# Performance work log

Measured on AMD Instinct MI355X. Metric: run time of the kernel, lower is better.

Reference implementation:

```python
import jax, jax.numpy as jnp
import numpy as np

NEG_SLOPE = 0.2  # PyG GATv2Conv default negative_slope


def _gatv2_layer(x, src, dst, Wl, Wr, att, bias, heads, out_ch, concat, num_nodes):
    # x: [N, F_in]; src/dst: [E'] (self-loops already appended)
    N, H, C = num_nodes, heads, out_ch
    xl = (x @ Wl).reshape(N, H, C)  # source-side transform (lin_l)
    xr = (x @ Wr).reshape(N, H, C)  # target-side transform (lin_r)
    m = xl[src] + xr[dst]                       # [E', H, C]
    e = jax.nn.leaky_relu(m, NEG_SLOPE)
    logits = jnp.einsum('ehc,hc->eh', e, att)   # [E', H]
    # numerically stable segment softmax over incoming edges of each dst node
    mx = jax.ops.segment_max(logits, dst, num_segments=N)   # [N, H]
    ex = jnp.exp(logits - mx[dst])
    den = jax.ops.segment_sum(ex, dst, num_segments=N)      # [N, H]
    alpha = ex / den[dst]                                    # [E', H]
    out = jax.ops.segment_sum(alpha[:, :, None] * xl[src], dst, num_segments=N)  # [N, H, C]
    out = out.reshape(N, H * C) if concat else out.mean(axis=1)
    return out + bias


def setup_inputs() -> dict:
    key = jax.random.key(0)
    N, E = 50000, 800000
    IN, HID, OUT, HEADS = 128, 32, 64, 4
    ks = jax.random.split(key, 16)
    x = jax.random.normal(ks[0], (N, IN), dtype=jnp.float32)
    edge_index = jax.random.randint(ks[1], (2, E), 0, N, dtype=jnp.int64)

    def lin(k, fin, fout):
        return jax.random.normal(k, (fin, fout), dtype=jnp.float32) * (1.0 / np.sqrt(fin))

    HC = HID * HEADS  # 128
    inp = {
        'x': x, 'edge_index': edge_index,
        # layer 1: IN -> HID x HEADS, concat
        'Wl1': lin(ks[2], IN, HC), 'Wr1': lin(ks[3], IN, HC),
        'a1': jax.random.normal(ks[4], (HEADS, HID), dtype=jnp.float32) * 0.1,
        'b1': jnp.zeros((HC,), dtype=jnp.float32),
        # layer 2: HC -> HID x HEADS, concat
        'Wl2': lin(ks[5], HC, HC), 'Wr2': lin(ks[6], HC, HC),
        'a2': jax.random.normal(ks[7], (HEADS, HID), dtype=jnp.float32) * 0.1,
        'b2': jnp.zeros((HC,), dtype=jnp.float32),
        # layer 3: HC -> OUT, heads=1, concat=False
        'Wl3': lin(ks[8], HC, OUT), 'Wr3': lin(ks[9], HC, OUT),
        'a3': jax.random.normal(ks[10], (1, OUT), dtype=jnp.float32) * 0.1,
        'b3': jnp.zeros((OUT,), dtype=jnp.float32),
    }
    return inp


def reference(x, edge_index, Wl1, Wr1, a1, b1, Wl2, Wr2, a2, b2, Wl3, Wr3, a3, b3):
    N = x.shape[0]
    # PyG GATv2Conv default add_self_loops=True
    loops = jnp.arange(N, dtype=edge_index.dtype)
    src = jnp.concatenate([edge_index[0], loops])
    dst = jnp.concatenate([edge_index[1], loops])
    HID, HEADS, OUT = 32, 4, 64
    h = _gatv2_layer(x, src, dst, Wl1, Wr1, a1, b1, HEADS, HID, True, N)
    h = jax.nn.elu(h)  # eval mode: dropout is identity
    h = _gatv2_layer(h, src, dst, Wl2, Wr2, a2, b2, HEADS, HID, True, N)
    h = jax.nn.elu(h)
    out = _gatv2_layer(h, src, dst, Wl3, Wr3, a3, b3, 1, OUT, False, N)
    return out
```

## Files before the change

### kernel.cpp

```cpp
#include <hip/hip_runtime.h>
#include <cstdint>
#include <cstddef>
#include <math.h>

#define NEG_SLOPE 0.2f
#define DEGB 512
#define EB 4096

typedef unsigned short ushort_t;
typedef __attribute__((ext_vector_type(8))) short short8;
typedef __attribute__((ext_vector_type(4))) float f32x4;
typedef _Float16 half8 __attribute__((ext_vector_type(8)));
typedef _Float16 half2_t __attribute__((ext_vector_type(2)));

__device__ __forceinline__ ushort_t f2bf(float f) {
    unsigned u = __float_as_uint(f);
    unsigned r = u + 0x7FFFu + ((u >> 16) & 1u);
    return (ushort_t)(r >> 16);
}
__device__ __forceinline__ float bf2f(ushort_t h) {
    return __uint_as_float(((unsigned)h) << 16);
}
__device__ __forceinline__ ushort_t f2h(float f) {
    _Float16 h = (_Float16)f;
    return *(ushort_t*)&h;
}

__device__ __forceinline__ float dot2acc(half2_t a, half2_t b, float c) {
#if __has_builtin(__builtin_amdgcn_fdot2)
    return __builtin_amdgcn_fdot2(a, b, c, false);
#else
    return c + (float)a[0] * (float)b[0] + (float)a[1] * (float)b[1];
#endif
}

template<int CTRL>
__device__ __forceinline__ float dpp_add(float p) {
    int t = __builtin_amdgcn_update_dpp(0, __builtin_bit_cast(int, p),
                                        CTRL, 0xF, 0xF, true);
    return p + __builtin_bit_cast(float, t);
}

__device__ __forceinline__ float swz4_add(float p) {
    int t = __builtin_amdgcn_ds_swizzle(__builtin_bit_cast(int, p), 0x101F);
    return p + __builtin_bit_cast(float, t);
}

__device__ __forceinline__ int wave_incl_scan(int v, int lane) {
    #pragma unroll
    for (int o = 1; o < 64; o <<= 1) {
        int t = __shfl_up(v, o, 64);
        if (lane >= o) v += t;
    }
    return v;
}


__global__ void bucket_hist(const int* __restrict__ ei, int E, int Et,
                            int* __restrict__ blkcnt) {
    __shared__ int cnt[256];
    int t = threadIdx.x;
    cnt[t] = 0;
    __syncthreads();
    int e0 = blockIdx.x * EB;
    #pragma unroll
    for (int it = 0; it < EB / 256; ++it) {
        int e = e0 + it * 256 + t;
        if (e < Et) {
            int d = (e < E) ? ei[E + e] : (e - E);
            atomicAdd(&cnt[d >> 8], 1);
        }
    }
    __syncthreads();
    blkcnt[blockIdx.x * 256 + t] = cnt[t];
}

__global__ void colscan(int* __restrict__ blkcnt, int nblk, int* __restrict__ btot) {
    int b = blockIdx.x;
    int lane = threadIdx.x;
    int running = 0;
    for (int base = 0; base < nblk; base += 64) {
        int idx = base + lane;
        int v = (idx < nblk) ? blkcnt[idx * 256 + b] : 0;
        int incl = wave_incl_scan(v, lane);
        if (idx < nblk) blkcnt[idx * 256 + b] = running + incl - v;
        running += __shfl(incl, 63, 64);
    }
    if (lane == 0) btot[b] = running;
}

__global__ void bucketscan(const int* __restrict__ btot, int* __restrict__ bbase) {
    __shared__ int tmp[256];
    int t = threadIdx.x;
    int v = btot[t];
    tmp[t] = v;
    __syncthreads();
    for (int o = 1; o < 256; o <<= 1) {
        int x = (t >= o) ? tmp[t - o] : 0;
        __syncthreads();
        tmp[t] += x;
        __syncthreads();
    }
    bbase[t] = tmp[t] - v;
}

__global__ void bucket_scatter(const int* __restrict__ ei, int E, int Et,
                               const int* __restrict__ blkrel,
                               const int* __restrict__ bbase,
                               unsigned* __restrict__ ebuf) {
    __shared__ int base_l[256];
    __shared__ int cnt[256];
    int t = threadIdx.x;
    base_l[t] = bbase[t] + blkrel[blockIdx.x * 256 + t];
    cnt[t] = 0;
    __syncthreads();
    int e0 = blockIdx.x * EB;
    #pragma unroll
    for (int it = 0; it < EB / 256; ++it) {
        int e = e0 + it * 256 + t;
        if (e < Et) {
            int s, d;
            if (e < E) { s = ei[e]; d = ei[E + e]; }
            else       { s = d = e - E; }
            int b = d >> 8;
            int r = atomicAdd(&cnt[b], 1);
            ebuf[base_l[b] + r] = (unsigned)s | (((unsigned)d & 255u) << 17);
        }
    }
}

__global__ void bucket_deg_scan_hist(const unsigned* __restrict__ ebuf,
                                     const int* __restrict__ bbase,
                                     const int* __restrict__ btot,
                                     int N, int* __restrict__ deg,
                                     int* __restrict__ rowstart,
                                     int* __restrict__ partials,
                                     int* __restrict__ dhist) {
    __shared__ int dcnt[256];
    __shared__ int tmp[256];
    __shared__ int h[DEGB];
    int b = blockIdx.x, t = threadIdx.x;
    dcnt[t] = 0;
    h[t] = 0; h[t + 256] = 0;
    __syncthreads();
    int s0 = bbase[b], c = btot[b];
    for (int i = t; i < c; i += 256)
        atomicAdd(&dcnt[ebuf[s0 + i] >> 17], 1);
    __syncthreads();
    int node = b * 256 + t;
    int dv = dcnt[t];
    if (node < N) deg[node] = dv;
    tmp[t] = dv;
    __syncthreads();
    for (int o = 1; o < 256; o <<= 1) {
        int x = (t >= o) ? tmp[t - o] : 0;
        __syncthreads();
        tmp[t] += x;
        __syncthreads();
    }
    if (node < N) rowstart[node] = tmp[t] - dv;
    if (t == 255) partials[b] = tmp[255];
    if (node < N) {
        int dc = dv < DEGB - 1 ? dv : DEGB - 1;
        atomicAdd(&h[dc], 1);
    }
    __syncthreads();
    int c0 = h[t];       if (c0) atomicAdd(&dhist[t], c0);
    int c1 = h[t + 256]; if (c1) atomicAdd(&dhist[t + 256], c1);
}

__global__ void finalize_scans(int* __restrict__ rowstart,
                               const int* __restrict__ partials, int nbkt, int N,
                               const int* __restrict__ dhist,
                               int* __restrict__ dstart) {
    __shared__ int tmp[DEGB];
    int t = threadIdx.x;
    int b = blockIdx.x;
    if (b < nbkt) {
        if (t < 256) tmp[t] = (t < nbkt) ? partials[t] : 0;
        __syncthreads();
        for (int o = 1; o < 256; o <<= 1) {
            int x = (t < 256 && t >= o) ? tmp[t - o] : 0;
            __syncthreads();
            if (t < 256) tmp[t] += x;
            __syncthreads();
        }
        int off = (b > 0) ? tmp[b - 1] : 0;
        int node = b * 256 + t;
        if (t < 256 && node < N) rowstart[node] += off;
    } else {
        int v = dhist[t];
        tmp[t] = v;
        __syncthreads();
        for (int o = 1; o < DEGB; o <<= 1) {
            int x = (t >= o) ? tmp[t - o] : 0;
            __syncthreads();
            tmp[t] += x;
            __syncthreads();
        }
        dstart[t] = tmp[DEGB - 1] - tmp[t];
    }
}

__global__ void csr_perm_scatter(const unsigned* __restrict__ ebuf,
                                 const int* __restrict__ bbase,
                                 const int* __restrict__ btot,
                                 const int* __restrict__ rowstart,
                                 const int* __restrict__ deg, int N,
                                 int* __restrict__ dstart,
                                 int* __restrict__ csr_src,
                                 int4* __restrict__ desc) {
    __shared__ int cur[256];
    __shared__ int h[DEGB];
    __shared__ int base[DEGB];
    int b = blockIdx.x, t = threadIdx.x;
    int node = b * 256 + t;
    int rs = (node < N) ? rowstart[node] : 0;
    cur[t] = rs;
    h[t] = 0; h[t + 256] = 0;
    __syncthreads();
    int s0 = bbase[b], c = btot[b];
    for (int i = t; i < c; i += 256) {
        unsigned v = ebuf[s0 + i];
        int pos = atomicAdd(&cur[v >> 17], 1);
        csr_src[pos] = (int)(v & 0x1FFFFu);
    }
    int dv = (node < N) ? deg[node] : 0;
    int dc = dv < DEGB - 1 ? dv : DEGB - 1;
    int r = 0;
    if (node < N) r = atomicAdd(&h[dc], 1);
    __syncthreads();
    int c0 = h[t];       if (c0) base[t]       = atomicAdd(&dstart[t], c0);
    int c1 = h[t + 256]; if (c1) base[t + 256] = atomicAdd(&dstart[t + 256], c1);
    __syncthreads();
    if (node < N) desc[base[dc] + r] = make_int4(node, rs, dv, 0);
}

template<int MOUT, bool CONVA>
__global__ __launch_bounds__(256) void gemm_mfma(const ushort_t* __restrict__ Ah,
                                                 const ushort_t* __restrict__ Al,
                                                 const float* __restrict__ Af,
                                                 const float* __restrict__ Wl,
                                                 const float* __restrict__ Wr,
                                                 ushort_t* __restrict__ xlh,
                                                 ushort_t* __restrict__ xrh, int N) {
    constexpr int NT  = MOUT / 16;
    constexpr int FPT = MOUT / 8;
    constexpr int CPR = MOUT / 4;
    __shared__ __align__(16) ushort_t Bh[NT * 2048];
    __shared__ __align__(16) ushort_t Bl[NT * 2048];
    const int tid   = threadIdx.x;
    const int row0  = blockIdx.x * 128;
    const bool isR  = blockIdx.y != 0;
    const float* W  = isR ? Wr : Wl;
    ushort_t* OUT   = isR ? xrh : xlh;

    #pragma unroll
    for (int i = 0; i < FPT; ++i) {
        int idx = tid * FPT + i;
        int k   = idx / CPR;
        int c4  = (idx % CPR) * 4;
        float4 w = *(const float4*)(W + (size_t)k * MOUT + c4);
        float wv[4] = {w.x, w.y, w.z, w.w};
        int q = k >> 5, quad = (k >> 3) & 3, j = k & 7;
        #pragma unroll
        for (int e = 0; e < 4; ++e) {
            int c = c4 + e;
            int t = c >> 4;
            int l = (quad << 4) | (c & 15);
            int pos = ((t * 4 + q) * 64 + l) * 8 + j;
            ushort_t hb = f2bf(wv[e]);
            Bh[pos] = hb;
            Bl[pos] = f2bf(wv[e] - bf2f(hb));
        }
    }
    __syncthreads();

    const int wv_  = tid >> 6;
    const int lane = tid & 63;
    const int m    = lane & 15;
    const int quad = lane >> 4;
    const int wrow0 = row0 + wv_ * 32;

    f32x4 acc[2][NT] = {};

    for (int q = 0; q < 4; ++q) {
        short8 ahf[2], alf[2];
        #pragma unroll
        for (int r = 0; r < 2; ++r) {
            int row = wrow0 + 16 * r + m;
            row = row < N ? row : N - 1;
            size_t off = (size_t)row * 128 + q * 32 + quad * 8;
            if constexpr (CONVA) {
                float4 f0 = *(const float4*)(Af + off);
                float4 f1 = *(const float4*)(Af + off + 4);
                float fv[8] = {f0.x, f0.y, f0.z, f0.w, f1.x, f1.y, f1.z, f1.w};
                short ah[8], al[8];
                #pragma unroll
                for (int e = 0; e < 8; ++e) {
                    ushort_t hb = f2bf(fv[e]);
                    ah[e] = (short)hb;
                    al[e] = (short)f2bf(fv[e] - bf2f(hb));
                }
                ahf[r] = short8{ah[0],ah[1],ah[2],ah[3],ah[4],ah[5],ah[6],ah[7]};
                alf[r] = short8{al[0],al[1],al[2],al[3],al[4],al[5],al[6],al[7]};
            } else {
                ahf[r] = *(const short8*)(Ah + off);
                alf[r] = *(const short8*)(Al + off);
            }
        }
        #pragma unroll
        for (int t = 0; t < NT; ++t) {
            int base = ((t * 4 + q) * 64 + lane) * 8;
            short8 bh = *(const short8*)(Bh + base);
            short8 bl = *(const short8*)(Bl + base);
            #pragma unroll
            for (int r = 0; r < 2; ++r) {
                acc[r][t] = __builtin_amdgcn_mfma_f32_16x16x32_bf16(ahf[r], bh, acc[r][t], 0, 0, 0);
                acc[r][t] = __builtin_amdgcn_mfma_f32_16x16x32_bf16(ahf[r], bl, acc[r][t], 0, 0, 0);
                acc[r][t] = __builtin_amdgcn_mfma_f32_16x16x32_bf16(alf[r], bh, acc[r][t], 0, 0, 0);
            }
        }
    }

    #pragma unroll
    for (int r = 0; r < 2; ++r)
        #pragma unroll
        for (int i = 0; i < 4; ++i) {
            int row = wrow0 + 16 * r + quad * 4 + i;
            if (row < N) {
                #pragma unroll
                for (int t = 0; t < NT; ++t)
                    OUT[(size_t)row * MOUT + t * 16 + m] = f2h(acc[r][t][i]);
            }
        }
}

template<int H, int C, bool ELU, int OMODE>
__global__ __launch_bounds__(512) void node_attn(const ushort_t* __restrict__ xlh,
                                                 const ushort_t* __restrict__ xrh,
                                                 const float* __restrict__ att,
                                                 const float* __restrict__ bias,
                                                 const int4* __restrict__ desc,
                                                 const int* __restrict__ csr_src,
                                                 int N, float* __restrict__ out,
                                                 ushort_t* __restrict__ outh,
                                                 ushort_t* __restrict__ outl) {
    constexpr int HC  = H * C;
    constexpr int VPT = 8;
    constexpr int LPG = HC / VPT;
    constexpr int GPW = 64 / LPG;
    constexpr int GROUP = C / VPT;
    constexpr int DR  = 5;

    const int lane = threadIdx.x & 63;
    const int wv   = threadIdx.x >> 6;
    const int gid  = lane / LPG;
    const int lig  = lane % LPG;
    const int ch0  = lig * VPT;

    const int s = (blockIdx.x * 8 + wv) * GPW + gid;
    if (s >= N) return;

    half2_t a2[4];
    {
        float4 u0 = *(const float4*)(att + ch0);
        float4 u1 = *(const float4*)(att + ch0 + 4);
        a2[0] = half2_t{(_Float16)u0.x, (_Float16)u0.y};
        a2[1] = half2_t{(_Float16)u0.z, (_Float16)u0.w};
        a2[2] = half2_t{(_Float16)u1.x, (_Float16)u1.y};
        a2[3] = half2_t{(_Float16)u1.z, (_Float16)u1.w};
    }
    float bias8[VPT];
    {
        float4 b0 = *(const float4*)(bias + ch0);
        float4 b1 = *(const float4*)(bias + ch0 + 4);
        bias8[0]=b0.x; bias8[1]=b0.y; bias8[2]=b0.z; bias8[3]=b0.w;
        bias8[4]=b1.x; bias8[5]=b1.y; bias8[6]=b1.z; bias8[7]=b1.w;
    }
    const half2_t c02 = half2_t{(_Float16)NEG_SLOPE, (_Float16)NEG_SLOPE};

    const int4 dsc = desc[s];
    const int n  = dsc.x;
    const int j0 = dsc.y;
    const int dg = dsc.z;

    half8 xrv = *(const half8*)(xrh + (size_t)n * HC + ch0);

    auto ldidx = [&](int e) {
        int ee = e < dg ? e : dg - 1;
        return csr_src[j0 + ee];
    };
    auto ldrow = [&](int idx) -> half8 {
        return *(const half8*)(xlh + (size_t)(unsigned)idx * HC + ch0);
    };

    float d = 0.f;
    float acc[VPT] = {};

    auto process = [&](half8 v) {
        float p = 0.f;
        #pragma unroll
        for (int i = 0; i < 4; ++i) {
            half2_t v2 = half2_t{v[2 * i], v[2 * i + 1]};
            half2_t x2 = half2_t{xrv[2 * i], xrv[2 * i + 1]};
            half2_t m2 = v2 + x2;
            half2_t lr = __builtin_elementwise_max(m2, c02 * m2);
            p = dot2acc(lr, a2[i], p);
        }
        if constexpr (GROUP >= 2) p = dpp_add<0xB1>(p);
        if constexpr (GROUP >= 4) p = dpp_add<0x4E>(p);
        if constexpr (GROUP >= 8) p = swz4_add(p);
        float pe = __expf(p);
        d += pe;
        #pragma unroll
        for (int i = 0; i < VPT; ++i)
            acc[i] += pe * (float)v[i];
    };

    int   ibuf[DR];
    half8 rbuf[DR];
    #pragma unroll
    for (int k = 0; k < DR; ++k) ibuf[k] = ldidx(k);
    #pragma unroll
    for (int k = 0; k < DR; ++k) {
        rbuf[k] = ldrow(ibuf[k]);
        ibuf[k] = ldidx(k + DR);
    }

    int e = 0;
    for (; e + DR <= dg; e += DR) {
        #pragma unroll
        for (int k = 0; k < DR; ++k) {
            half8 v = rbuf[k];
            rbuf[k] = ldrow(ibuf[k]);
            ibuf[k] = ldidx(e + k + 2 * DR);
            process(v);
        }
    }
    #pragma unroll
    for (int k = 0; k < DR; ++k)
        if (e + k < dg) process(rbuf[k]);

    float inv = 1.f / d;
    float vv[VPT];
    #pragma unroll
    for (int i = 0; i < VPT; ++i) {
        float v = acc[i] * inv + bias8[i];
        if (ELU) v = v > 0.f ? v : (__expf(v) - 1.f);
        vv[i] = v;
    }
    if (OMODE == 0) {
        *(float4*)(out + (size_t)n * HC + ch0) =
            make_float4(vv[0], vv[1], vv[2], vv[3]);
        *(float4*)(out + (size_t)n * HC + ch0 + 4) =
            make_float4(vv[4], vv[5], vv[6], vv[7]);
    } else {
        ushort_t hb[VPT], lb[VPT];
        #pragma unroll
        for (int i = 0; i < VPT; ++i) {
            hb[i] = f2bf(vv[i]);
            lb[i] = f2bf(vv[i] - bf2f(hb[i]));
        }
        *(ushort4*)(outh + (size_t)n * HC + ch0) =
            ushort4{hb[0], hb[1], hb[2], hb[3]};
        *(ushort4*)(outh + (size_t)n * HC + ch0 + 4) =
            ushort4{hb[4], hb[5], hb[6], hb[7]};
        *(ushort4*)(outl + (size_t)n * HC + ch0) =
            ushort4{lb[0], lb[1], lb[2], lb[3]};
        *(ushort4*)(outl + (size_t)n * HC + ch0 + 4) =
            ushort4{lb[4], lb[5], lb[6], lb[7]};
    }
}

extern "C" void kernel_launch(void* const* d_in, const int* in_sizes, int n_in,
                              void* d_out, int out_size, void* d_ws, size_t ws_size,
                              hipStream_t stream) {
    const float* x   = (const float*)d_in[0];
    const int*   ei  = (const int*)d_in[1];
    const float* Wl1 = (const float*)d_in[2];
    const float* Wr1 = (const float*)d_in[3];
    const float* a1  = (const float*)d_in[4];
    const float* b1  = (const float*)d_in[5];
    const float* Wl2 = (const float*)d_in[6];
    const float* Wr2 = (const float*)d_in[7];
    const float* a2  = (const float*)d_in[8];
    const float* b2  = (const float*)d_in[9];
    const float* Wl3 = (const float*)d_in[10];
    const float* Wr3 = (const float*)d_in[11];
    const float* a3  = (const float*)d_in[12];
    const float* b3  = (const float*)d_in[13];

    const int N  = in_sizes[0] / 128;
    const int E  = in_sizes[1] / 2;
    const int Et = E + N;
    const int nb = (N + 255) / 256;

    char* p = (char*)d_ws;
    auto alloc = [&](size_t bytes) -> void* {
        void* r = (void*)p;
        p += (bytes + 255) & ~(size_t)255;
        return r;
    };
    const int ebBlocks = (Et + EB - 1) / EB;
    int*      csr_src  = (int*)alloc((size_t)Et * 4 + 256);
    unsigned* ebuf     = (unsigned*)alloc((size_t)Et * 4);
    int*      blkcnt   = (int*)alloc((size_t)ebBlocks * 256 * 4);
    int*      btot     = (int*)alloc(256 * 4);
    int*      bbase    = (int*)alloc(256 * 4);
    int*      deg      = (int*)alloc((size_t)N * 4);
    int*      rowstart = (int*)alloc((size_t)N * 4);
    int*      partials = (int*)alloc((size_t)nb * 4);
    int4*     desc     = (int4*)alloc((size_t)N * 16);
    int*      dhist    = (int*)alloc((size_t)DEGB * 4);
    int*      dstart   = (int*)alloc((size_t)DEGB * 4);
    ushort_t* xlh      = (ushort_t*)alloc((size_t)N * 128 * 2);
    ushort_t* xrh      = (ushort_t*)alloc((size_t)N * 128 * 2);
    ushort_t* Ah       = (ushort_t*)alloc((size_t)N * 128 * 2);
    ushort_t* Al       = (ushort_t*)alloc((size_t)N * 128 * 2);

    const int rowBlocks    = (N + 127) / 128;
    const int nodeBlocks12 = (N + 31) / 32;
    const int nodeBlocks3  = (N + 63) / 64;

    hipMemsetAsync(dhist, 0, (size_t)DEGB * 4, stream);
    bucket_hist<<<ebBlocks, 256, 0, stream>>>(ei, E, Et, blkcnt);
    colscan<<<256, 64, 0, stream>>>(blkcnt, ebBlocks, btot);
    bucketscan<<<1, 256, 0, stream>>>(btot, bbase);
    bucket_scatter<<<ebBlocks, 256, 0, stream>>>(ei, E, Et, blkcnt, bbase, ebuf);
    bucket_deg_scan_hist<<<nb, 256, 0, stream>>>(ebuf, bbase, btot, N,
                                                 deg, rowstart, partials, dhist);
    finalize_scans<<<nb + 1, DEGB, 0, stream>>>(rowstart, partials, nb, N,
                                                dhist, dstart);
    csr_perm_scatter<<<nb, 256, 0, stream>>>(ebuf, bbase, btot, rowstart, deg, N,
                                             dstart, csr_src, desc);

    gemm_mfma<128, true><<<dim3(rowBlocks, 2), 256, 0, stream>>>(
        nullptr, nullptr, x, Wl1, Wr1, xlh, xrh, N);
    node_attn<4, 32, true, 1><<<nodeBlocks12, 512, 0, stream>>>(
        xlh, xrh, a1, b1, desc, csr_src, N, nullptr, Ah, Al);

    gemm_mfma<128, false><<<dim3(rowBlocks, 2), 256, 0, stream>>>(
        Ah, Al, nullptr, Wl2, Wr2, xlh, xrh, N);
    node_attn<4, 32, true, 1><<<nodeBlocks12, 512, 0, stream>>>(
        xlh, xrh, a2, b2, desc, csr_src, N, nullptr, Ah, Al);

    float* out = (float*)d_out;
    gemm_mfma<64, false><<<dim3(rowBlocks, 2), 256, 0, stream>>>(
        Ah, Al, nullptr, Wl3, Wr3, xlh, xrh, N);
    node_attn<1, 64, false, 0><<<nodeBlocks3, 512, 0, stream>>>(
        xlh, xrh, a3, b3, desc, csr_src, N, out, nullptr, nullptr);
}
```

Measured before the change: 286.5 us.

## Fuse edge bucket histogram into first GEMM launch and drop memset

The bucket histogram kernel becomes extra leading blocks of the layer-1 GEMM launch, so the histogram work and the x@W transform share one grid. The degree-histogram memset moves into colscan. This removes two launches and a memset, and lets the histogram overlap with the GEMM. The GEMM grid becomes one-dimensional, with the left/right choice taken from the block index parity. The cost is a branch at block entry and shared-memory reuse for the counters.

```diff
diff --git a/kernel.cpp b/kernel.cpp
--- a/kernel.cpp
+++ b/kernel.cpp
@@ -56,28 +56,11 @@
 }
 
 
-__global__ void bucket_hist(const int* __restrict__ ei, int E, int Et,
-                            int* __restrict__ blkcnt) {
-    __shared__ int cnt[256];
-    int t = threadIdx.x;
-    cnt[t] = 0;
-    __syncthreads();
-    int e0 = blockIdx.x * EB;
-    #pragma unroll
-    for (int it = 0; it < EB / 256; ++it) {
-        int e = e0 + it * 256 + t;
-        if (e < Et) {
-            int d = (e < E) ? ei[E + e] : (e - E);
-            atomicAdd(&cnt[d >> 8], 1);
-        }
-    }
-    __syncthreads();
-    blkcnt[blockIdx.x * 256 + t] = cnt[t];
-}
-
-__global__ void colscan(int* __restrict__ blkcnt, int nblk, int* __restrict__ btot) {
+__global__ void colscan(int* __restrict__ blkcnt, int nblk, int* __restrict__ btot,
+                        int* __restrict__ dhist) {
     int b = blockIdx.x;
     int lane = threadIdx.x;
+    if (lane < 2) dhist[b * 2 + lane] = 0;
     int running = 0;
     for (int base = 0; base < nblk; base += 64) {
         int idx = base + lane;
@@ -243,15 +226,39 @@
                                                  const float* __restrict__ Wl,
                                                  const float* __restrict__ Wr,
                                                  ushort_t* __restrict__ xlh,
-                                                 ushort_t* __restrict__ xrh, int N) {
+                                                 ushort_t* __restrict__ xrh, int N,
+                                                 const int* __restrict__ ei,
+                                                 int E, int Et,
+                                                 int* __restrict__ blkcnt,
+                                                 int histBlocks) {
     constexpr int NT  = MOUT / 16;
     constexpr int FPT = MOUT / 8;
     constexpr int CPR = MOUT / 4;
     __shared__ __align__(16) ushort_t Bh[NT * 2048];
     __shared__ __align__(16) ushort_t Bl[NT * 2048];
-    const int tid   = threadIdx.x;
-    const int row0  = blockIdx.x * 128;
-    const bool isR  = blockIdx.y != 0;
+    const int tid = threadIdx.x;
+
+    if ((int)blockIdx.x < histBlocks) {
+        int* cnt = (int*)Bh;
+        cnt[tid] = 0;
+        __syncthreads();
+        int e0 = blockIdx.x * EB;
+        #pragma unroll
+        for (int it = 0; it < EB / 256; ++it) {
+            int e = e0 + it * 256 + tid;
+            if (e < Et) {
+                int d = (e < E) ? ei[E + e] : (e - E);
+                atomicAdd(&cnt[d >> 8], 1);
+            }
+        }
+        __syncthreads();
+        blkcnt[blockIdx.x * 256 + tid] = cnt[tid];
+        return;
+    }
+
+    const int g     = (int)blockIdx.x - histBlocks;
+    const int row0  = (g >> 1) * 128;
+    const bool isR  = (g & 1) != 0;
     const float* W  = isR ? Wr : Wl;
     ushort_t* OUT   = isR ? xrh : xlh;
 
@@ -523,9 +530,10 @@
     const int nodeBlocks12 = (N + 31) / 32;
     const int nodeBlocks3  = (N + 63) / 64;
 
-    hipMemsetAsync(dhist, 0, (size_t)DEGB * 4, stream);
-    bucket_hist<<<ebBlocks, 256, 0, stream>>>(ei, E, Et, blkcnt);
-    colscan<<<256, 64, 0, stream>>>(blkcnt, ebBlocks, btot);
+    gemm_mfma<128, true><<<ebBlocks + rowBlocks * 2, 256, 0, stream>>>(
+        nullptr, nullptr, x, Wl1, Wr1, xlh, xrh, N, ei, E, Et, blkcnt, ebBlocks);
+
+    colscan<<<256, 64, 0, stream>>>(blkcnt, ebBlocks, btot, dhist);
     bucketscan<<<1, 256, 0, stream>>>(btot, bbase);
     bucket_scatter<<<ebBlocks, 256, 0, stream>>>(ei, E, Et, blkcnt, bbase, ebuf);
     bucket_deg_scan_hist<<<nb, 256, 0, stream>>>(ebuf, bbase, btot, N,
@@ -535,19 +543,17 @@
     csr_perm_scatter<<<nb, 256, 0, stream>>>(ebuf, bbase, btot, rowstart, deg, N,
                                              dstart, csr_src, desc);
 
-    gemm_mfma<128, true><<<dim3(rowBlocks, 2), 256, 0, stream>>>(
-        nullptr, nullptr, x, Wl1, Wr1, xlh, xrh, N);
     node_attn<4, 32, true, 1><<<nodeBlocks12, 512, 0, stream>>>(
         xlh, xrh, a1, b1, desc, csr_src, N, nullptr, Ah, Al);
 
-    gemm_mfma<128, false><<<dim3(rowBlocks, 2), 256, 0, stream>>>(
-        Ah, Al, nullptr, Wl2, Wr2, xlh, xrh, N);
+    gemm_mfma<128, false><<<rowBlocks * 2, 256, 0, stream>>>(
+        Ah, Al, nullptr, Wl2, Wr2, xlh, xrh, N, nullptr, 0, 0, nullptr, 0);
     node_attn<4, 32, true, 1><<<nodeBlocks12, 512, 0, stream>>>(
         xlh, xrh, a2, b2, desc, csr_src, N, nullptr, Ah, Al);
 
     float* out = (float*)d_out;
-    gemm_mfma<64, false><<<dim3(rowBlocks, 2), 256, 0, stream>>>(
-        Ah, Al, nullptr, Wl3, Wr3, xlh, xrh, N);
+    gemm_mfma<64, false><<<rowBlocks * 2, 256, 0, stream>>>(
+        Ah, Al, nullptr, Wl3, Wr3, xlh, xrh, N, nullptr, 0, 0, nullptr, 0);
     node_attn<1, 64, false, 0><<<nodeBlocks3, 512, 0, stream>>>(
         xlh, xrh, a3, b3, desc, csr_src, N, out, nullptr, nullptr);
 }
```

Result: faster. 280.5 us (-2.1%).
